# Kernel optimization log

Measured on AMD Instinct MI355X. Metric: run time of the kernel, lower is better.

The kernel has to match this reference:

```python
import jax, jax.numpy as jnp
import numpy as np

N = 50000      # nodes
E = 800000     # edges (avg degree 16)
G = 8          # graphs in batch
D = 128        # in/hidden feats
C = 10         # classes


def setup_inputs() -> dict:
    key = jax.random.key(0)
    ks = jax.random.split(key, 9)
    x = jax.random.normal(ks[0], (N, D), dtype=jnp.float32)
    edge_index = jax.random.randint(ks[1], (2, E), 0, N)
    node2graph = jnp.sort(jax.random.randint(ks[2], (N,), 0, G))
    s = 1.0 / np.sqrt(D)
    W1 = jax.random.normal(ks[3], (D, D), dtype=jnp.float32) * s
    b1 = jnp.zeros((D,), jnp.float32)
    W2 = jax.random.normal(ks[4], (D, D), dtype=jnp.float32) * s
    b2 = jnp.zeros((D,), jnp.float32)
    Wl = jax.random.normal(ks[5], (D, C), dtype=jnp.float32) * s
    bl = jnp.zeros((C,), jnp.float32)
    return {"x": x, "edge_index": edge_index, "node2graph": node2graph,
            "W1": W1, "b1": b1, "W2": W2, "b2": b2, "Wl": Wl, "bl": bl}


def _graph_conv(h, src, dst, out_isqrt, in_isqrt, W, b):
    # DGL GraphConv, norm='both': D_in^{-1/2} A D_out^{-1/2} (h W) + b
    h = (h * out_isqrt[:, None]) @ W
    agg = jax.ops.segment_sum(h[src], dst, num_segments=N)  # SpMM gather/scatter
    return agg * in_isqrt[:, None] + b


def reference(x, edge_index, node2graph, W1, b1, W2, b2, Wl, bl):
    src, dst = edge_index[0], edge_index[1]
    ones_e = jnp.ones((E,), jnp.float32)
    out_deg = jnp.clip(jax.ops.segment_sum(ones_e, src, num_segments=N), 1.0)
    in_deg = jnp.clip(jax.ops.segment_sum(ones_e, dst, num_segments=N), 1.0)
    out_isqrt = jax.lax.rsqrt(out_deg)
    in_isqrt = jax.lax.rsqrt(in_deg)

    h = jax.nn.relu(_graph_conv(x, src, dst, out_isqrt, in_isqrt, W1, b1))
    h = jax.nn.relu(_graph_conv(h, src, dst, out_isqrt, in_isqrt, W2, b2))

    # AvgPooling: per-graph mean of node features
    sums = jax.ops.segment_sum(h, node2graph, num_segments=G)
    counts = jnp.clip(jax.ops.segment_sum(jnp.ones((N,), jnp.float32), node2graph, num_segments=G), 1.0)
    hg = sums / counts[:, None]

    logits = hg @ Wl + bl
    return jax.nn.softmax(logits, axis=1)
```

## Files before the change

kernel.cpp:

```cpp
#include <hip/hip_runtime.h>
#include <stdint.h>

#define FD 128
#define NG 8
#define NC 10
#define MAXB 1024
#define CHUNK 4096
#define BFPAD 4

typedef __attribute__((ext_vector_type(8))) short bf16x8;
typedef __attribute__((ext_vector_type(4))) float f32x4;
typedef __attribute__((ext_vector_type(2))) float f32x2;

__device__ __forceinline__ float bf2f(uint16_t u){
    union { uint32_t i; float f; } v; v.i = ((uint32_t)u) << 16; return v.f;
}
__device__ __forceinline__ uint16_t f2bf(float f){
    union { float f; uint32_t i; } v; v.f = f;
    uint32_t r = v.i + 0x7fff + ((v.i >> 16) & 1);
    return (uint16_t)(r >> 16);
}

#if __has_builtin(__builtin_amdgcn_cvt_pk_f32_fp8) && __has_builtin(__builtin_amdgcn_cvt_pk_fp8_f32)
__device__ __forceinline__ f32x2 fp8lo2f(uint32_t p){
    return __builtin_amdgcn_cvt_pk_f32_fp8((int)p, false);
}
__device__ __forceinline__ f32x2 fp8hi2f(uint32_t p){
    return __builtin_amdgcn_cvt_pk_f32_fp8((int)p, true);
}
__device__ __forceinline__ uint32_t pk4fp8(float a, float b, float c, float d){
    int u = 0;
    u = __builtin_amdgcn_cvt_pk_fp8_f32(a, b, u, false);
    u = __builtin_amdgcn_cvt_pk_fp8_f32(c, d, u, true);
    return (uint32_t)u;
}
#else
__device__ __forceinline__ float fp8tof(uint32_t b){
    union { uint32_t i; float f; } v;
    v.i = ((b & 0x7f) << 20) | ((b & 0x80) << 24);
    return v.f * 0x1p120f;
}
__device__ __forceinline__ f32x2 fp8lo2f(uint32_t p){
    return (f32x2){fp8tof(p & 0xff), fp8tof((p >> 8) & 0xff)};
}
__device__ __forceinline__ f32x2 fp8hi2f(uint32_t p){
    return (f32x2){fp8tof((p >> 16) & 0xff), fp8tof((p >> 24) & 0xff)};
}
__device__ __forceinline__ uint32_t f2fp8(float f){
    union { float f; uint32_t i; } v; v.f = f;
    uint32_t s = (v.i >> 24) & 0x80;
    float a = fabsf(f);
    if (a < 0x1p-10f) return s;
    if (a > 448.f) return s | 0x7e;
    v.f = a;
    uint32_t r = v.i + 0x7ffff + ((v.i >> 20) & 1);
    int e = (int)(r >> 23) - 127 + 7;
    uint32_t m = (r >> 20) & 7;
    if (e <= 0){
        uint32_t q = (uint32_t)(a * 512.f + 0.5f);
        return s | (q > 7 ? 8 : q);
    }
    if (e > 15) return s | 0x7e;
    return s | ((uint32_t)e << 3) | m;
}
__device__ __forceinline__ uint32_t pk4fp8(float a, float b, float c, float d){
    return (uint32_t)f2fp8(a) | ((uint32_t)f2fp8(b)<<8) |
           ((uint32_t)f2fp8(c)<<16) | ((uint32_t)f2fp8(d)<<24);
}
#endif

__global__ __launch_bounds__(256) void k_prep(const float* __restrict__ W1,
        const float* __restrict__ W2, uint16_t* Wf1, uint16_t* Wf2,
        int B, int* __restrict__ bfD, int* __restrict__ bfS,
        float* __restrict__ pool){
    int t = threadIdx.x;
    int id = blockIdx.x*256 + t;
    {
        int w = id >> 14;
        int r = id & 16383;
        int j = r & 7, frag = r >> 3;
        int lane = frag & 63, t2 = frag >> 6;
        int n = t2 & 7, kk = t2 >> 3;
        int k = kk*32 + (lane>>4)*8 + j;
        int col = n*16 + (lane&15);
        float v = (w ? W2 : W1)[k*128 + col];
        (w ? Wf2 : Wf1)[r] = f2bf(v);
    }
    for (int i = id; i < B*BFPAD; i += 32768){ bfD[i] = 0; bfS[i] = 0; }
    if (id < NG*FD) pool[id] = 0.f;
}

__global__ __launch_bounds__(1024) void k_gemm_scatter(const int* __restrict__ ei,
        int E, int B, int shift, int CAP, int C,
        int* __restrict__ bfD, int* __restrict__ bfS,
        uint32_t* __restrict__ tempD, uint16_t* __restrict__ tempS,
        const float* __restrict__ X, const uint16_t* __restrict__ Wf,
        uint8_t* __restrict__ out8, int N){
    __shared__ __align__(16) char lds[45056];
    int t = threadIdx.x;
    int lmask = (1<<shift) - 1;
    if ((int)blockIdx.x < C){
        uint32_t* pay = (uint32_t*)lds;
        int* cnt  = (int*)(lds + 7168*4);
        int* off  = cnt  + MAXB;
        int* resv = off  + MAXB;
        int* scr  = resv + MAXB;
        for (int i=t;i<7168;i+=1024) pay[i] = 0xFFFFFFFFu;
        for (int i=t;i<B;i+=1024) cnt[i] = 0;
        __syncthreads();
        int c = blockIdx.x;
        int e0 = c*CHUNK, e1 = min(E, e0+CHUNK);
        int bb[4], pl[4]; uint32_t val[4];
        #pragma unroll
        for (int k=0;k<4;k++){
            int e = e0 + t + k*1024;
            bb[k] = -1;
            if (e < e1){
                int s = ei[e], d = ei[E+e];
                int b = d >> shift;
                bb[k] = b; val[k] = ((uint32_t)(d & lmask) << 20) | (uint32_t)s;
                pl[k] = atomicAdd(&cnt[b], 1);
            }
        }
        __syncthreads();
        int v = (t < B) ? ((cnt[t]+3) & ~3) : 0;
        scr[t] = v; __syncthreads();
        for (int o=1;o<1024;o<<=1){ int u=(t>=o)?scr[t-o]:0; __syncthreads(); scr[t]+=u; __syncthreads(); }
        if (t < B) off[t] = scr[t] - v;
        __syncthreads();
        int totalPad = scr[1023];
        #pragma unroll
        for (int k=0;k<4;k++)
            if (bb[k] >= 0) pay[off[bb[k]] + pl[k]] = val[k];
        for (int b=t;b<B;b+=1024){
            int pc = (cnt[b]+3) & ~3;
            resv[b] = pc ? atomicAdd(&bfD[b*BFPAD], pc) : 0;
        }
        __syncthreads();
        for (int g=t; g < (totalPad>>2); g += 1024){
            int pos = g << 2;
            int lo = 0, hi = B-1;
            while (lo < hi){ int mid=(lo+hi+1)>>1; if (off[mid] <= pos) lo = mid; else hi = mid-1; }
            int rel = resv[lo] + (pos - off[lo]);
            if (rel + 4 <= CAP){
                uint4 w4 = *(const uint4*)&pay[pos];
                *(uint4*)&tempD[(size_t)lo*CAP + rel] = w4;
            }
        }
        return;
    }
    if ((int)blockIdx.x < 2*C){
        uint16_t* pay = (uint16_t*)lds;
        int* cnt  = (int*)(lds + 11264*2);
        int* off  = cnt  + MAXB;
        int* resv = off  + MAXB;
        int* scr  = resv + MAXB;
        for (int i=t;i<11264;i+=1024) pay[i] = 0xFFFF;
        for (int i=t;i<B;i+=1024) cnt[i] = 0;
        __syncthreads();
        int c = blockIdx.x - C;
        int e0 = c*CHUNK, e1 = min(E, e0+CHUNK);
        int bb[4], pl[4]; uint16_t val[4];
        #pragma unroll
        for (int k=0;k<4;k++){
            int e = e0 + t + k*1024;
            bb[k] = -1;
            if (e < e1){
                int s = ei[e];
                int b = s >> shift;
                bb[k] = b; val[k] = (uint16_t)(s & lmask);
                pl[k] = atomicAdd(&cnt[b], 1);
            }
        }
        __syncthreads();
        int v = (t < B) ? ((cnt[t]+7) & ~7) : 0;
        scr[t] = v; __syncthreads();
        for (int o=1;o<1024;o<<=1){ int u=(t>=o)?scr[t-o]:0; __syncthreads(); scr[t]+=u; __syncthreads(); }
        if (t < B) off[t] = scr[t] - v;
        __syncthreads();
        int totalPad = scr[1023];
        #pragma unroll
        for (int k=0;k<4;k++)
            if (bb[k] >= 0) pay[off[bb[k]] + pl[k]] = val[k];
        for (int b=t;b<B;b+=1024){
            int pc = (cnt[b]+7) & ~7;
            resv[b] = pc ? atomicAdd(&bfS[b*BFPAD], pc) : 0;
        }
        __syncthreads();
        for (int g=t; g < (totalPad>>3); g += 1024){
            int pos = g << 3;
            int lo = 0, hi = B-1;
            while (lo < hi){ int mid=(lo+hi+1)>>1; if (off[mid] <= pos) lo = mid; else hi = mid-1; }
            int rel = resv[lo] + (pos - off[lo]);
            if (rel + 8 <= CAP){
                uint4 w4 = *(const uint4*)&pay[pos];
                *(uint4*)&tempS[(size_t)lo*CAP + rel] = w4;
            }
        }
        return;
    }
    int wave = t>>6, lane = t&63, quad = lane>>4, low = lane&15;
    int rowA  = (blockIdx.x - 2*C)*256 + wave*16 + low;
    int rowAc = min(rowA, N-1);
    const float* arow = X + (size_t)rowAc*FD;
    bf16x8 ah[4];
    #pragma unroll
    for (int kk=0;kk<4;kk++){
        f32x4 f0 = *(const f32x4*)(arow + kk*32 + quad*8);
        f32x4 f1 = *(const f32x4*)(arow + kk*32 + quad*8 + 4);
        #pragma unroll
        for (int j=0;j<4;j++) ah[kk][j]   = (short)f2bf(f0[j]);
        #pragma unroll
        for (int j=0;j<4;j++) ah[kk][j+4] = (short)f2bf(f1[j]);
    }
    f32x4 acc[8];
    #pragma unroll
    for (int n=0;n<8;n++) acc[n] = (f32x4){0.f,0.f,0.f,0.f};
    #pragma unroll
    for (int kk=0;kk<4;kk++){
        #pragma unroll
        for (int n=0;n<8;n++){
            bf16x8 bh = *(const bf16x8*)(Wf + ((size_t)((kk*8+n)*64 + lane))*8);
            acc[n] = __builtin_amdgcn_mfma_f32_16x16x32_bf16(bh, ah[kk], acc[n], 0, 0, 0);
        }
    }
    if (rowA < N){
        uint8_t* orow = out8 + (size_t)rowA*FD;
        #pragma unroll
        for (int n=0;n<8;n++){
            uint32_t pk = pk4fp8(acc[n][0], acc[n][1], acc[n][2], acc[n][3]);
            *(uint32_t*)(orow + n*16 + quad*4) = pk;
        }
    }
}

__global__ __launch_bounds__(256) void k_build(const uint32_t* __restrict__ tempD,
        const uint16_t* __restrict__ tempS,
        const int* __restrict__ bfD, const int* __restrict__ bfS,
        int B, int shift, int N, int CAP,
        int* __restrict__ row_off, int* __restrict__ deg_in,
        float* __restrict__ isqo, int* __restrict__ csr){
    __shared__ int cnt_[MAXB];
    __shared__ int off_[MAXB];
    int b = blockIdx.x, t = threadIdx.x;
    int range = 1<<shift, nb0 = b<<shift;
    int fill = min(bfD[b*BFPAD], CAP);
    const uint32_t* seg = tempD + (size_t)b*CAP;
    for (int i=t;i<range;i+=256) cnt_[i]=0;
    __syncthreads();
    for (int i=t;i<fill;i+=256){
        int loc = (int)(seg[i] >> 20);
        if (loc < range) atomicAdd(&cnt_[loc], 1);
    }
    __syncthreads();
    if (range == 64){
        if (t < 64){
            int v = cnt_[t];
            int inc = v;
            #pragma unroll
            for (int o=1;o<64;o<<=1){
                int u = __shfl_up(inc, o);
                if (t >= o) inc += u;
            }
            off_[t] = inc - v;
        }
    } else if (t == 0){
        int run = 0;
        for (int i=0;i<range;i++){ off_[i]=run; run+=cnt_[i]; }
    }
    __syncthreads();
    int base = b*CAP;
    for (int i=t;i<range;i+=256){
        int node = nb0 + i;
        if (node < N){
            row_off[node] = base + off_[i];
            deg_in[node]  = cnt_[i];
        }
    }
    __syncthreads();
    int* csrb = csr + (size_t)base;
    for (int i=t;i<fill;i+=256){
        uint32_t v = seg[i];
        int loc = (int)(v >> 20);
        if (loc < range){
            int p = atomicAdd(&off_[loc], 1);
            csrb[p] = (int)(v & 0xFFFFFu);
        }
    }
    __syncthreads();
    for (int i=t;i<range;i+=256) cnt_[i]=0;
    __syncthreads();
    int fillS = min(bfS[b*BFPAD], CAP);
    const uint16_t* segS = tempS + (size_t)b*CAP;
    for (int i=t;i<fillS;i+=256){
        int v = (int)segS[i];
        if (v < range) atomicAdd(&cnt_[v], 1);
    }
    __syncthreads();
    for (int i=t;i<range;i+=256){
        int node = nb0 + i;
        if (node < N) isqo[node] = rsqrtf((float)max(cnt_[i], 1));
    }
}

template<bool WSCALE>
__device__ __forceinline__ void spmm_row(const uint2* __restrict__ tp,
        const int* __restrict__ csr_src, const float* __restrict__ isqo,
        int e0, int e1, int l, int qb,
        f32x2& a01, f32x2& a23, f32x2& a45, f32x2& a67){
    for (int base = e0; base < e1; base += 16){
        int my = 0;
        if (base + l < e1) my = csr_src[base + l];
        int cnt = min(16, e1 - base);
        for (int j0 = 0; j0 < cnt; j0 += 8){
            int ss[8];
            #pragma unroll
            for (int k=0;k<8;k++)
                ss[k] = __shfl(my, qb + min(j0 + k, cnt-1));
            uint2 p[8]; float w[8];
            #pragma unroll
            for (int k=0;k<8;k++)
                p[k] = tp[(size_t)ss[k]*16 + l];
            if (WSCALE){
                #pragma unroll
                for (int k=0;k<8;k++) w[k] = isqo[ss[k]];
            }
            #pragma unroll
            for (int k=0;k<8;k++){
                if (j0 + k < cnt){
                    if (WSCALE){
                        a01 += fp8lo2f(p[k].x)*w[k]; a23 += fp8hi2f(p[k].x)*w[k];
                        a45 += fp8lo2f(p[k].y)*w[k]; a67 += fp8hi2f(p[k].y)*w[k];
                    } else {
                        a01 += fp8lo2f(p[k].x); a23 += fp8hi2f(p[k].x);
                        a45 += fp8lo2f(p[k].y); a67 += fp8hi2f(p[k].y);
                    }
                }
            }
        }
    }
}

__global__ __launch_bounds__(256) void k_spmm_gemm(const uint8_t* __restrict__ tmp8,
        const int* __restrict__ row_off, const int* __restrict__ deg_in,
        const int* __restrict__ csr_src, const float* __restrict__ isqo,
        const float* __restrict__ bias, const uint16_t* __restrict__ Wf,
        uint8_t* __restrict__ out8, int N){
    __shared__ __align__(16) uint16_t hsrow[64][136];
    int tid = threadIdx.x;
    int l = tid & 15, qid = tid >> 4, qb = (tid & 63) & 48;
    const uint2* tp = (const uint2*)tmp8;
    f32x4 bv0 = *(const f32x4*)(bias + l*8);
    f32x4 bv1 = *(const f32x4*)(bias + l*8 + 4);
    #pragma unroll
    for (int i = 0; i < 4; i++){
        int rowL = qid*4 + i;
        int node = blockIdx.x*64 + rowL;
        int e0 = 0, e1 = 0;
        if (node < N){ e0 = row_off[node]; e1 = e0 + deg_in[node]; }
        f32x2 a01={0.f,0.f}, a23={0.f,0.f}, a45={0.f,0.f}, a67={0.f,0.f};
        spmm_row<true>(tp, csr_src, isqo, e0, e1, l, qb, a01, a23, a45, a67);
        float isq = rsqrtf((float)max(e1 - e0, 1));
        float r0 = fmaxf(a01.x*isq + bv0[0], 0.f);
        float r1 = fmaxf(a01.y*isq + bv0[1], 0.f);
        float r2 = fmaxf(a23.x*isq + bv0[2], 0.f);
        float r3 = fmaxf(a23.y*isq + bv0[3], 0.f);
        float r4 = fmaxf(a45.x*isq + bv1[0], 0.f);
        float r5 = fmaxf(a45.y*isq + bv1[1], 0.f);
        float r6 = fmaxf(a67.x*isq + bv1[2], 0.f);
        float r7 = fmaxf(a67.y*isq + bv1[3], 0.f);
        uint4 o;
        o.x = (uint32_t)f2bf(r0) | ((uint32_t)f2bf(r1) << 16);
        o.y = (uint32_t)f2bf(r2) | ((uint32_t)f2bf(r3) << 16);
        o.z = (uint32_t)f2bf(r4) | ((uint32_t)f2bf(r5) << 16);
        o.w = (uint32_t)f2bf(r6) | ((uint32_t)f2bf(r7) << 16);
        if (node >= N) o = (uint4){0u,0u,0u,0u};
        *(uint4*)(&hsrow[rowL][l*8]) = o;
    }
    __syncthreads();
    int wave = tid>>6, lane = tid&63, quad = lane>>4, low = lane&15;
    int rowL = wave*16 + low;
    int rowA = blockIdx.x*64 + rowL;
    bf16x8 ah[4];
    #pragma unroll
    for (int kk=0;kk<4;kk++)
        ah[kk] = *(const bf16x8*)(&hsrow[rowL][kk*32 + quad*8]);
    f32x4 acc[8];
    #pragma unroll
    for (int n=0;n<8;n++) acc[n] = (f32x4){0.f,0.f,0.f,0.f};
    #pragma unroll
    for (int kk=0;kk<4;kk++){
        #pragma unroll
        for (int n=0;n<8;n++){
            bf16x8 bh = *(const bf16x8*)(Wf + ((size_t)((kk*8+n)*64 + lane))*8);
            acc[n] = __builtin_amdgcn_mfma_f32_16x16x32_bf16(bh, ah[kk], acc[n], 0, 0, 0);
        }
    }
    if (rowA < N){
        float sc = isqo[rowA];
        uint8_t* orow = out8 + (size_t)rowA*FD;
        #pragma unroll
        for (int n=0;n<8;n++){
            uint32_t pk = pk4fp8(acc[n][0]*sc, acc[n][1]*sc, acc[n][2]*sc, acc[n][3]*sc);
            *(uint32_t*)(orow + n*16 + quad*4) = pk;
        }
    }
}

__global__ __launch_bounds__(256) void k_spmm_pool(const uint8_t* __restrict__ tmp8,
        const int* __restrict__ row_off, const int* __restrict__ deg_in,
        const int* __restrict__ csr_src,
        const float* __restrict__ bias, const int* __restrict__ n2g,
        float* __restrict__ pool, int N){
    __shared__ float sacc[NG*FD];
    int tid = threadIdx.x;
    for (int i = tid; i < NG*FD; i += 256) sacc[i] = 0.f;
    __syncthreads();
    int l = tid & 15, qid = tid >> 4, qb = (tid & 63) & 48;
    const uint2* tp = (const uint2*)tmp8;
    f32x4 bv0 = *(const f32x4*)(bias + l*8);
    f32x4 bv1 = *(const f32x4*)(bias + l*8 + 4);
    int rg = -1;
    float racc[8];
    #pragma unroll
    for (int j=0;j<8;j++) racc[j] = 0.f;
    #pragma unroll
    for (int i = 0; i < 4; i++){
        int node = blockIdx.x*64 + qid*4 + i;
        if (node < N){
            int e0 = row_off[node], e1 = e0 + deg_in[node];
            f32x2 a01={0.f,0.f}, a23={0.f,0.f}, a45={0.f,0.f}, a67={0.f,0.f};
            spmm_row<false>(tp, csr_src, nullptr, e0, e1, l, qb, a01, a23, a45, a67);
            float isq = rsqrtf((float)max(e1 - e0, 1));
            float r[8];
            r[0] = fmaxf(a01.x*isq + bv0[0], 0.f);
            r[1] = fmaxf(a01.y*isq + bv0[1], 0.f);
            r[2] = fmaxf(a23.x*isq + bv0[2], 0.f);
            r[3] = fmaxf(a23.y*isq + bv0[3], 0.f);
            r[4] = fmaxf(a45.x*isq + bv1[0], 0.f);
            r[5] = fmaxf(a45.y*isq + bv1[1], 0.f);
            r[6] = fmaxf(a67.x*isq + bv1[2], 0.f);
            r[7] = fmaxf(a67.y*isq + bv1[3], 0.f);
            int g = n2g[node];
            if (g != rg){
                if (rg >= 0){
                    #pragma unroll
                    for (int j=0;j<8;j++) atomicAdd(&sacc[rg*FD + l*8 + j], racc[j]);
                }
                rg = g;
                #pragma unroll
                for (int j=0;j<8;j++) racc[j] = 0.f;
            }
            #pragma unroll
            for (int j=0;j<8;j++) racc[j] += r[j];
        }
    }
    if (rg >= 0){
        #pragma unroll
        for (int j=0;j<8;j++) atomicAdd(&sacc[rg*FD + l*8 + j], racc[j]);
    }
    __syncthreads();
    for (int i = tid; i < NG*FD; i += 256){
        float v = sacc[i];
        if (v != 0.f) atomicAdd(&pool[i], v);
    }
}

__global__ __launch_bounds__(128) void k_final(const float* __restrict__ pool,
        const int* __restrict__ n2g, int N, const float* __restrict__ Wl,
        const float* __restrict__ bl, float* __restrict__ out){
    __shared__ int ub[NG+1];
    __shared__ float logits[NG][NC];
    int t = threadIdx.x;
    if (t <= NG){
        int lo = 0, hi = N;
        while (lo < hi){ int mid = (lo+hi)>>1; if (n2g[mid] < t) lo = mid+1; else hi = mid; }
        ub[t] = lo;
    }
    __syncthreads();
    if (t < NG*NC){
        int g = t/NC, c = t%NC;
        float cnt = (float)max(ub[g+1]-ub[g], 1);
        float inv = 1.f/cnt;
        float acc = bl[c];
        for (int d=0; d<FD; d++)
            acc += pool[g*FD+d]*inv * Wl[d*NC+c];
        logits[g][c] = acc;
    }
    __syncthreads();
    if (t < NG*NC){
        int g = t/NC, c = t%NC;
        float m = -1e30f;
        for (int i=0;i<NC;i++) m = fmaxf(m, logits[g][i]);
        float ssum = 0.f;
        for (int i=0;i<NC;i++) ssum += expf(logits[g][i]-m);
        out[t] = expf(logits[g][c]-m)/ssum;
    }
}

extern "C" void kernel_launch(void* const* d_in, const int* in_sizes, int n_in,
                              void* d_out, int out_size, void* d_ws, size_t ws_size,
                              hipStream_t stream) {
    const float* x   = (const float*)d_in[0];
    const int*   ei  = (const int*)d_in[1];
    const int*   n2g = (const int*)d_in[2];
    const float* W1  = (const float*)d_in[3];
    const float* b1  = (const float*)d_in[4];
    const float* W2  = (const float*)d_in[5];
    const float* b2  = (const float*)d_in[6];
    const float* Wl  = (const float*)d_in[7];
    const float* bl  = (const float*)d_in[8];
    float* outp = (float*)d_out;

    int N = in_sizes[2];
    int E = in_sizes[1] / 2;

    int shift = 6;
    while ((((N + (1<<shift) - 1) >> shift) > MAXB) && shift < 10) shift++;
    int B = (N + (1<<shift) - 1) >> shift;
    int C = (E + CHUNK - 1) / CHUNK;
    int meanFill = (int)(((long long)E << shift) / (N > 0 ? N : 1)) + 1;
    int CAP = 4096;
    while (CAP < 3*meanFill) CAP <<= 1;

    char* w = (char*)d_ws;
    size_t off = 0;
    auto alloc = [&](size_t bytes)->char*{ char* p = w + off; off += (bytes + 255) & ~(size_t)255; return p; };
    float*    pool    = (float*)alloc((size_t)NG*FD*4);
    int*      deg_in  = (int*)alloc((size_t)N*4);
    int*      row_off = (int*)alloc((size_t)N*4);
    float*    isqo    = (float*)alloc((size_t)N*4);
    int*      bfD     = (int*)alloc((size_t)MAXB*BFPAD*4);
    int*      bfS     = (int*)alloc((size_t)MAXB*BFPAD*4);
    uint16_t* Wf1     = (uint16_t*)alloc(16384*2);
    uint16_t* Wf2     = (uint16_t*)alloc(16384*2);
    uint32_t* tempD   = (uint32_t*)alloc((size_t)B*CAP*4);
    uint16_t* tempS   = (uint16_t*)alloc((size_t)B*CAP*2);
    int*      csr     = (int*)alloc((size_t)B*CAP*4);
    uint8_t*  tmp8    = (uint8_t*)alloc((size_t)N*FD);
    uint8_t*  tmp8b   = (uint8_t*)alloc((size_t)N*FD);
    (void)ws_size;

    int gb2 = (N + 255)/256;
    int gb  = (N + 63)/64;

    k_prep        <<<128,         256,  0, stream>>>(W1, W2, Wf1, Wf2, B, bfD, bfS, pool);
    k_gemm_scatter<<<2*C + gb2,   1024, 0, stream>>>(ei, E, B, shift, CAP, C,
                                                     bfD, bfS, tempD, tempS,
                                                     x, Wf1, tmp8, N);
    k_build       <<<B,           256,  0, stream>>>(tempD, tempS, bfD, bfS, B, shift, N, CAP,
                                                     row_off, deg_in, isqo, csr);
    k_spmm_gemm   <<<gb,          256,  0, stream>>>(tmp8,  row_off, deg_in, csr, isqo, b1, Wf2, tmp8b, N);
    k_spmm_pool   <<<gb,          256,  0, stream>>>(tmp8b, row_off, deg_in, csr, b2, n2g, pool, N);
    k_final       <<<1,           128,  0, stream>>>(pool, n2g, N, Wl, bl, outp);
}
```

Measured before the change: 197.9 us.

## Quantize intermediate node features to per-row scaled FP4 for SpMM gathers

Stores the transformed node features as 4-bit E2M1 values with a per-row scale instead of FP8. This halves the bytes gathered per edge in both SpMM passes, and the per-row scale is folded into per-node weight tables (wtab1/wtab2) used during aggregation. The SpMM kernels also drop from 64 to 32 rows per block, with occupancy hints, and the second GEMM splits output columns across waves, using an LDS atomicMax to find each row's maximum. The cost is much coarser quantization and some extra encode/decode ALU work, which risks accuracy.

```diff
diff --git a/kernel.cpp b/kernel.cpp
--- a/kernel.cpp
+++ b/kernel.cpp
@@ -21,51 +21,35 @@
     return (uint16_t)(r >> 16);
 }
 
-#if __has_builtin(__builtin_amdgcn_cvt_pk_f32_fp8) && __has_builtin(__builtin_amdgcn_cvt_pk_fp8_f32)
-__device__ __forceinline__ f32x2 fp8lo2f(uint32_t p){
-    return __builtin_amdgcn_cvt_pk_f32_fp8((int)p, false);
-}
-__device__ __forceinline__ f32x2 fp8hi2f(uint32_t p){
-    return __builtin_amdgcn_cvt_pk_f32_fp8((int)p, true);
-}
-__device__ __forceinline__ uint32_t pk4fp8(float a, float b, float c, float d){
-    int u = 0;
-    u = __builtin_amdgcn_cvt_pk_fp8_f32(a, b, u, false);
-    u = __builtin_amdgcn_cvt_pk_fp8_f32(c, d, u, true);
-    return (uint32_t)u;
+__device__ __forceinline__ uint32_t enc4(float v, float s){
+    float a = fabsf(v)*s;
+    uint32_t c = (uint32_t)((a>=0.25f)+(a>=0.75f)+(a>=1.25f)+(a>=1.75f)
+                           +(a>=2.5f)+(a>=3.5f)+(a>=5.f));
+    return c | ((__float_as_uint(v)>>28) & 8u);
+}
+#if __has_builtin(__builtin_amdgcn_cvt_scalef32_pk_f32_fp4)
+__device__ __forceinline__ void acc_fp4(uint32_t p, float w,
+        f32x2& a01, f32x2& a23, f32x2& a45, f32x2& a67){
+    f32x2 d;
+    d = __builtin_amdgcn_cvt_scalef32_pk_f32_fp4(p, 1.0f, 0); a01.x += d.x*w; a01.y += d.y*w;
+    d = __builtin_amdgcn_cvt_scalef32_pk_f32_fp4(p, 1.0f, 1); a23.x += d.x*w; a23.y += d.y*w;
+    d = __builtin_amdgcn_cvt_scalef32_pk_f32_fp4(p, 1.0f, 2); a45.x += d.x*w; a45.y += d.y*w;
+    d = __builtin_amdgcn_cvt_scalef32_pk_f32_fp4(p, 1.0f, 3); a67.x += d.x*w; a67.y += d.y*w;
 }
 #else
-__device__ __forceinline__ float fp8tof(uint32_t b){
-    union { uint32_t i; float f; } v;
-    v.i = ((b & 0x7f) << 20) | ((b & 0x80) << 24);
-    return v.f * 0x1p120f;
-}
-__device__ __forceinline__ f32x2 fp8lo2f(uint32_t p){
-    return (f32x2){fp8tof(p & 0xff), fp8tof((p >> 8) & 0xff)};
-}
-__device__ __forceinline__ f32x2 fp8hi2f(uint32_t p){
-    return (f32x2){fp8tof((p >> 16) & 0xff), fp8tof((p >> 24) & 0xff)};
-}
-__device__ __forceinline__ uint32_t f2fp8(float f){
-    union { float f; uint32_t i; } v; v.f = f;
-    uint32_t s = (v.i >> 24) & 0x80;
-    float a = fabsf(f);
-    if (a < 0x1p-10f) return s;
-    if (a > 448.f) return s | 0x7e;
-    v.f = a;
-    uint32_t r = v.i + 0x7ffff + ((v.i >> 20) & 1);
-    int e = (int)(r >> 23) - 127 + 7;
-    uint32_t m = (r >> 20) & 7;
-    if (e <= 0){
-        uint32_t q = (uint32_t)(a * 512.f + 0.5f);
-        return s | (q > 7 ? 8 : q);
-    }
-    if (e > 15) return s | 0x7e;
-    return s | ((uint32_t)e << 3) | m;
-}
-__device__ __forceinline__ uint32_t pk4fp8(float a, float b, float c, float d){
-    return (uint32_t)f2fp8(a) | ((uint32_t)f2fp8(b)<<8) |
-           ((uint32_t)f2fp8(c)<<16) | ((uint32_t)f2fp8(d)<<24);
+__device__ __forceinline__ float dec4(uint32_t n, float w){
+    uint32_t c = n & 7u;
+    uint32_t bits = (c >= 2u) ? (0x3F000000u + (c << 22)) : ((c & 1u) ? 0x3F000000u : 0u);
+    bits |= (n & 8u) << 28;
+    union { uint32_t u; float f; } v; v.u = bits;
+    return v.f * w;
+}
+__device__ __forceinline__ void acc_fp4(uint32_t p, float w,
+        f32x2& a01, f32x2& a23, f32x2& a45, f32x2& a67){
+    a01.x += dec4(p & 15u, w);        a01.y += dec4((p>>4) & 15u, w);
+    a23.x += dec4((p>>8) & 15u, w);   a23.y += dec4((p>>12) & 15u, w);
+    a45.x += dec4((p>>16) & 15u, w);  a45.y += dec4((p>>20) & 15u, w);
+    a67.x += dec4((p>>24) & 15u, w);  a67.y += dec4(p>>28, w);
 }
 #endif
 
@@ -95,7 +79,7 @@
         int* __restrict__ bfD, int* __restrict__ bfS,
         uint32_t* __restrict__ tempD, uint16_t* __restrict__ tempS,
         const float* __restrict__ X, const uint16_t* __restrict__ Wf,
-        uint8_t* __restrict__ out8, int N){
+        uint8_t* __restrict__ out4, float* __restrict__ rsc1, int N){
     __shared__ __align__(16) char lds[45056];
     int t = threadIdx.x;
     int lmask = (1<<shift) - 1;
@@ -224,13 +208,24 @@
             acc[n] = __builtin_amdgcn_mfma_f32_16x16x32_bf16(bh, ah[kk], acc[n], 0, 0, 0);
         }
     }
+    float m = 0.f;
+    #pragma unroll
+    for (int n=0;n<8;n++){
+        #pragma unroll
+        for (int j=0;j<4;j++) m = fmaxf(m, fabsf(acc[n][j]));
+    }
+    m = fmaxf(m, __shfl_xor(m, 16));
+    m = fmaxf(m, __shfl_xor(m, 32));
+    float s = (m > 0.f) ? 6.f/m : 0.f;
     if (rowA < N){
-        uint8_t* orow = out8 + (size_t)rowA*FD;
+        uint8_t* orow = out4 + (size_t)rowA*64;
         #pragma unroll
         for (int n=0;n<8;n++){
-            uint32_t pk = pk4fp8(acc[n][0], acc[n][1], acc[n][2], acc[n][3]);
-            *(uint32_t*)(orow + n*16 + quad*4) = pk;
-        }
+            uint32_t h = enc4(acc[n][0],s) | (enc4(acc[n][1],s)<<4)
+                       | (enc4(acc[n][2],s)<<8) | (enc4(acc[n][3],s)<<12);
+            *(uint16_t*)(orow + n*8 + quad*2) = (uint16_t)h;
+        }
+        if (quad == 0) rsc1[rowA] = m * (1.f/6.f);
     }
 }
 
@@ -239,7 +234,9 @@
         const int* __restrict__ bfD, const int* __restrict__ bfS,
         int B, int shift, int N, int CAP,
         int* __restrict__ row_off, int* __restrict__ deg_in,
-        float* __restrict__ isqo, int* __restrict__ csr){
+        const float* __restrict__ rsc1,
+        float* __restrict__ isqo, float* __restrict__ wtab1,
+        int* __restrict__ csr){
     __shared__ int cnt_[MAXB];
     __shared__ int off_[MAXB];
     int b = blockIdx.x, t = threadIdx.x;
@@ -299,13 +296,16 @@
     __syncthreads();
     for (int i=t;i<range;i+=256){
         int node = nb0 + i;
-        if (node < N) isqo[node] = rsqrtf((float)max(cnt_[i], 1));
-    }
-}
-
-template<bool WSCALE>
-__device__ __forceinline__ void spmm_row(const uint2* __restrict__ tp,
-        const int* __restrict__ csr_src, const float* __restrict__ isqo,
+        if (node < N){
+            float iq = rsqrtf((float)max(cnt_[i], 1));
+            isqo[node]  = iq;
+            wtab1[node] = iq * rsc1[node];
+        }
+    }
+}
+
+__device__ __forceinline__ void spmm_row4(const uint32_t* __restrict__ tp,
+        const int* __restrict__ csr_src, const float* __restrict__ wt,
         int e0, int e1, int l, int qb,
         f32x2& a01, f32x2& a23, f32x2& a45, f32x2& a67){
     for (int base = e0; base < e1; base += 16){
@@ -317,49 +317,44 @@
             #pragma unroll
             for (int k=0;k<8;k++)
                 ss[k] = __shfl(my, qb + min(j0 + k, cnt-1));
-            uint2 p[8]; float w[8];
+            uint32_t p[8]; float w[8];
             #pragma unroll
             for (int k=0;k<8;k++)
                 p[k] = tp[(size_t)ss[k]*16 + l];
-            if (WSCALE){
-                #pragma unroll
-                for (int k=0;k<8;k++) w[k] = isqo[ss[k]];
-            }
+            #pragma unroll
+            for (int k=0;k<8;k++)
+                w[k] = wt[ss[k]];
             #pragma unroll
             for (int k=0;k<8;k++){
-                if (j0 + k < cnt){
-                    if (WSCALE){
-                        a01 += fp8lo2f(p[k].x)*w[k]; a23 += fp8hi2f(p[k].x)*w[k];
-                        a45 += fp8lo2f(p[k].y)*w[k]; a67 += fp8hi2f(p[k].y)*w[k];
-                    } else {
-                        a01 += fp8lo2f(p[k].x); a23 += fp8hi2f(p[k].x);
-                        a45 += fp8lo2f(p[k].y); a67 += fp8hi2f(p[k].y);
-                    }
-                }
-            }
-        }
-    }
-}
-
-__global__ __launch_bounds__(256) void k_spmm_gemm(const uint8_t* __restrict__ tmp8,
+                if (j0 + k < cnt)
+                    acc_fp4(p[k], w[k], a01, a23, a45, a67);
+            }
+        }
+    }
+}
+
+__global__ __launch_bounds__(256, 6) void k_spmm_gemm(const uint8_t* __restrict__ tmp4a,
         const int* __restrict__ row_off, const int* __restrict__ deg_in,
-        const int* __restrict__ csr_src, const float* __restrict__ isqo,
+        const int* __restrict__ csr_src, const float* __restrict__ wtab1,
+        const float* __restrict__ isqo,
         const float* __restrict__ bias, const uint16_t* __restrict__ Wf,
-        uint8_t* __restrict__ out8, int N){
-    __shared__ __align__(16) uint16_t hsrow[64][136];
+        uint8_t* __restrict__ out4, float* __restrict__ wtab2, int N){
+    __shared__ __align__(16) uint16_t hsrow[32][136];
+    __shared__ uint32_t rmax[32];
     int tid = threadIdx.x;
+    if (tid < 32) rmax[tid] = 0u;
     int l = tid & 15, qid = tid >> 4, qb = (tid & 63) & 48;
-    const uint2* tp = (const uint2*)tmp8;
+    const uint32_t* tp = (const uint32_t*)tmp4a;
     f32x4 bv0 = *(const f32x4*)(bias + l*8);
     f32x4 bv1 = *(const f32x4*)(bias + l*8 + 4);
     #pragma unroll
-    for (int i = 0; i < 4; i++){
-        int rowL = qid*4 + i;
-        int node = blockIdx.x*64 + rowL;
+    for (int i = 0; i < 2; i++){
+        int rowL = qid*2 + i;
+        int node = blockIdx.x*32 + rowL;
         int e0 = 0, e1 = 0;
         if (node < N){ e0 = row_off[node]; e1 = e0 + deg_in[node]; }
         f32x2 a01={0.f,0.f}, a23={0.f,0.f}, a45={0.f,0.f}, a67={0.f,0.f};
-        spmm_row<true>(tp, csr_src, isqo, e0, e1, l, qb, a01, a23, a45, a67);
+        spmm_row4(tp, csr_src, wtab1, e0, e1, l, qb, a01, a23, a45, a67);
         float isq = rsqrtf((float)max(e1 - e0, 1));
         float r0 = fmaxf(a01.x*isq + bv0[0], 0.f);
         float r1 = fmaxf(a01.y*isq + bv0[1], 0.f);
@@ -379,37 +374,51 @@
     }
     __syncthreads();
     int wave = tid>>6, lane = tid&63, quad = lane>>4, low = lane&15;
-    int rowL = wave*16 + low;
-    int rowA = blockIdx.x*64 + rowL;
+    int rowL = (wave&1)*16 + low;
+    int rowA = blockIdx.x*32 + rowL;
+    int nb0 = (wave>>1)*4;
     bf16x8 ah[4];
     #pragma unroll
     for (int kk=0;kk<4;kk++)
         ah[kk] = *(const bf16x8*)(&hsrow[rowL][kk*32 + quad*8]);
-    f32x4 acc[8];
-    #pragma unroll
-    for (int n=0;n<8;n++) acc[n] = (f32x4){0.f,0.f,0.f,0.f};
+    f32x4 acc[4];
+    #pragma unroll
+    for (int n=0;n<4;n++) acc[n] = (f32x4){0.f,0.f,0.f,0.f};
     #pragma unroll
     for (int kk=0;kk<4;kk++){
         #pragma unroll
-        for (int n=0;n<8;n++){
+        for (int n2=0;n2<4;n2++){
+            int n = nb0 + n2;
             bf16x8 bh = *(const bf16x8*)(Wf + ((size_t)((kk*8+n)*64 + lane))*8);
-            acc[n] = __builtin_amdgcn_mfma_f32_16x16x32_bf16(bh, ah[kk], acc[n], 0, 0, 0);
-        }
-    }
+            acc[n2] = __builtin_amdgcn_mfma_f32_16x16x32_bf16(bh, ah[kk], acc[n2], 0, 0, 0);
+        }
+    }
+    float pm = 0.f;
+    #pragma unroll
+    for (int n2=0;n2<4;n2++){
+        #pragma unroll
+        for (int j=0;j<4;j++) pm = fmaxf(pm, fabsf(acc[n2][j]));
+    }
+    atomicMax(&rmax[rowL], __float_as_uint(pm));
+    __syncthreads();
+    float m = __uint_as_float(rmax[rowL]);
+    float s = (m > 0.f) ? 6.f/m : 0.f;
     if (rowA < N){
-        float sc = isqo[rowA];
-        uint8_t* orow = out8 + (size_t)rowA*FD;
-        #pragma unroll
-        for (int n=0;n<8;n++){
-            uint32_t pk = pk4fp8(acc[n][0]*sc, acc[n][1]*sc, acc[n][2]*sc, acc[n][3]*sc);
-            *(uint32_t*)(orow + n*16 + quad*4) = pk;
-        }
-    }
-}
-
-__global__ __launch_bounds__(256) void k_spmm_pool(const uint8_t* __restrict__ tmp8,
+        uint8_t* orow = out4 + (size_t)rowA*64;
+        #pragma unroll
+        for (int n2=0;n2<4;n2++){
+            int n = nb0 + n2;
+            uint32_t h = enc4(acc[n2][0],s) | (enc4(acc[n2][1],s)<<4)
+                       | (enc4(acc[n2][2],s)<<8) | (enc4(acc[n2][3],s)<<12);
+            *(uint16_t*)(orow + n*8 + quad*2) = (uint16_t)h;
+        }
+        if (nb0 == 0 && quad == 0) wtab2[rowA] = isqo[rowA] * m * (1.f/6.f);
+    }
+}
+
+__global__ __launch_bounds__(256, 6) void k_spmm_pool(const uint8_t* __restrict__ tmp4b,
         const int* __restrict__ row_off, const int* __restrict__ deg_in,
-        const int* __restrict__ csr_src,
+        const int* __restrict__ csr_src, const float* __restrict__ wtab2,
         const float* __restrict__ bias, const int* __restrict__ n2g,
         float* __restrict__ pool, int N){
     __shared__ float sacc[NG*FD];
@@ -417,7 +426,7 @@
     for (int i = tid; i < NG*FD; i += 256) sacc[i] = 0.f;
     __syncthreads();
     int l = tid & 15, qid = tid >> 4, qb = (tid & 63) & 48;
-    const uint2* tp = (const uint2*)tmp8;
+    const uint32_t* tp = (const uint32_t*)tmp4b;
     f32x4 bv0 = *(const f32x4*)(bias + l*8);
     f32x4 bv1 = *(const f32x4*)(bias + l*8 + 4);
     int rg = -1;
@@ -425,12 +434,12 @@
     #pragma unroll
     for (int j=0;j<8;j++) racc[j] = 0.f;
     #pragma unroll
-    for (int i = 0; i < 4; i++){
-        int node = blockIdx.x*64 + qid*4 + i;
+    for (int i = 0; i < 2; i++){
+        int node = blockIdx.x*32 + qid*2 + i;
         if (node < N){
             int e0 = row_off[node], e1 = e0 + deg_in[node];
             f32x2 a01={0.f,0.f}, a23={0.f,0.f}, a45={0.f,0.f}, a67={0.f,0.f};
-            spmm_row<false>(tp, csr_src, nullptr, e0, e1, l, qb, a01, a23, a45, a67);
+            spmm_row4(tp, csr_src, wtab2, e0, e1, l, qb, a01, a23, a45, a67);
             float isq = rsqrtf((float)max(e1 - e0, 1));
             float r[8];
             r[0] = fmaxf(a01.x*isq + bv0[0], 0.f);
@@ -530,6 +539,9 @@
     int*      deg_in  = (int*)alloc((size_t)N*4);
     int*      row_off = (int*)alloc((size_t)N*4);
     float*    isqo    = (float*)alloc((size_t)N*4);
+    float*    rsc1    = (float*)alloc((size_t)N*4);
+    float*    wtab1   = (float*)alloc((size_t)N*4);
+    float*    wtab2   = (float*)alloc((size_t)N*4);
     int*      bfD     = (int*)alloc((size_t)MAXB*BFPAD*4);
     int*      bfS     = (int*)alloc((size_t)MAXB*BFPAD*4);
     uint16_t* Wf1     = (uint16_t*)alloc(16384*2);
@@ -537,20 +549,22 @@
     uint32_t* tempD   = (uint32_t*)alloc((size_t)B*CAP*4);
     uint16_t* tempS   = (uint16_t*)alloc((size_t)B*CAP*2);
     int*      csr     = (int*)alloc((size_t)B*CAP*4);
-    uint8_t*  tmp8    = (uint8_t*)alloc((size_t)N*FD);
-    uint8_t*  tmp8b   = (uint8_t*)alloc((size_t)N*FD);
+    uint8_t*  tmp4a   = (uint8_t*)alloc((size_t)N*64);
+    uint8_t*  tmp4b   = (uint8_t*)alloc((size_t)N*64);
     (void)ws_size;
 
     int gb2 = (N + 255)/256;
-    int gb  = (N + 63)/64;
+    int gb  = (N + 31)/32;
 
     k_prep        <<<128,         256,  0, stream>>>(W1, W2, Wf1, Wf2, B, bfD, bfS, pool);
     k_gemm_scatter<<<2*C + gb2,   1024, 0, stream>>>(ei, E, B, shift, CAP, C,
                                                      bfD, bfS, tempD, tempS,
-                                                     x, Wf1, tmp8, N);
+                                                     x, Wf1, tmp4a, rsc1, N);
     k_build       <<<B,           256,  0, stream>>>(tempD, tempS, bfD, bfS, B, shift, N, CAP,
-                                                     row_off, deg_in, isqo, csr);
-    k_spmm_gemm   <<<gb,          256,  0, stream>>>(tmp8,  row_off, deg_in, csr, isqo, b1, Wf2, tmp8b, N);
-    k_spmm_pool   <<<gb,          256,  0, stream>>>(tmp8b, row_off, deg_in, csr, b2, n2g, pool, N);
+                                                     row_off, deg_in, rsc1, isqo, wtab1, csr);
+    k_spmm_gemm   <<<gb,          256,  0, stream>>>(tmp4a, row_off, deg_in, csr, wtab1, isqo,
+                                                     b1, Wf2, tmp4b, wtab2, N);
+    k_spmm_pool   <<<gb,          256,  0, stream>>>(tmp4b, row_off, deg_in, csr, wtab2,
+                                                     b2, n2g, pool, N);
     k_final       <<<1,           128,  0, stream>>>(pool, n2g, N, Wl, bl, outp);
 }
```

Measured after the change: 195.4 us. About the same (-1.3%).

## Merge dst/src bucketing blocks and halve rows per SpMM block

Applied to the files above, without the earlier changes.

The scatter kernel now has each edge-chunk block load src and dst once and run both the dst bucketing and the src bucketing passes in sequence, reusing the LDS. This halves the number of bucketing blocks and avoids reading the edge list twice. Separately, the SpMM+GEMM and SpMM+pool kernels now handle 32 nodes per block instead of 64. In the fused GEMM stage each wave computes half of the output columns, and both kernels get an occupancy hint of 6. The aim is more blocks and better latency hiding for the gather, at the cost of serialising the two bucketing passes inside each block.

```diff
diff --git a/kernel.cpp b/kernel.cpp
--- a/kernel.cpp
+++ b/kernel.cpp
@@ -100,25 +100,32 @@
     int t = threadIdx.x;
     int lmask = (1<<shift) - 1;
     if ((int)blockIdx.x < C){
-        uint32_t* pay = (uint32_t*)lds;
-        int* cnt  = (int*)(lds + 7168*4);
+        uint32_t* payD = (uint32_t*)lds;
+        uint16_t* payS = (uint16_t*)lds;
+        int* cnt  = (int*)(lds + 28672);
         int* off  = cnt  + MAXB;
         int* resv = off  + MAXB;
         int* scr  = resv + MAXB;
-        for (int i=t;i<7168;i+=1024) pay[i] = 0xFFFFFFFFu;
-        for (int i=t;i<B;i+=1024) cnt[i] = 0;
-        __syncthreads();
         int c = blockIdx.x;
         int e0 = c*CHUNK, e1 = min(E, e0+CHUNK);
-        int bb[4], pl[4]; uint32_t val[4];
+        int ss[4], dd[4];
         #pragma unroll
         for (int k=0;k<4;k++){
             int e = e0 + t + k*1024;
+            bool ok = e < e1;
+            ss[k] = ok ? ei[e]   : -1;
+            dd[k] = ok ? ei[E+e] : -1;
+        }
+        for (int i=t;i<7168;i+=1024) payD[i] = 0xFFFFFFFFu;
+        for (int i=t;i<B;i+=1024) cnt[i] = 0;
+        __syncthreads();
+        int bb[4], pl[4];
+        #pragma unroll
+        for (int k=0;k<4;k++){
             bb[k] = -1;
-            if (e < e1){
-                int s = ei[e], d = ei[E+e];
-                int b = d >> shift;
-                bb[k] = b; val[k] = ((uint32_t)(d & lmask) << 20) | (uint32_t)s;
+            if (dd[k] >= 0){
+                int b = dd[k] >> shift;
+                bb[k] = b;
                 pl[k] = atomicAdd(&cnt[b], 1);
             }
         }
@@ -131,7 +138,8 @@
         int totalPad = scr[1023];
         #pragma unroll
         for (int k=0;k<4;k++)
-            if (bb[k] >= 0) pay[off[bb[k]] + pl[k]] = val[k];
+            if (bb[k] >= 0)
+                payD[off[bb[k]] + pl[k]] = ((uint32_t)(dd[k] & lmask) << 20) | (uint32_t)ss[k];
         for (int b=t;b<B;b+=1024){
             int pc = (cnt[b]+3) & ~3;
             resv[b] = pc ? atomicAdd(&bfD[b*BFPAD], pc) : 0;
@@ -143,45 +151,33 @@
             while (lo < hi){ int mid=(lo+hi+1)>>1; if (off[mid] <= pos) lo = mid; else hi = mid-1; }
             int rel = resv[lo] + (pos - off[lo]);
             if (rel + 4 <= CAP){
-                uint4 w4 = *(const uint4*)&pay[pos];
+                uint4 w4 = *(const uint4*)&payD[pos];
                 *(uint4*)&tempD[(size_t)lo*CAP + rel] = w4;
             }
         }
-        return;
-    }
-    if ((int)blockIdx.x < 2*C){
-        uint16_t* pay = (uint16_t*)lds;
-        int* cnt  = (int*)(lds + 11264*2);
-        int* off  = cnt  + MAXB;
-        int* resv = off  + MAXB;
-        int* scr  = resv + MAXB;
-        for (int i=t;i<11264;i+=1024) pay[i] = 0xFFFF;
+        __syncthreads();
+        for (int i=t;i<11264;i+=1024) payS[i] = 0xFFFF;
         for (int i=t;i<B;i+=1024) cnt[i] = 0;
         __syncthreads();
-        int c = blockIdx.x - C;
-        int e0 = c*CHUNK, e1 = min(E, e0+CHUNK);
-        int bb[4], pl[4]; uint16_t val[4];
         #pragma unroll
         for (int k=0;k<4;k++){
-            int e = e0 + t + k*1024;
             bb[k] = -1;
-            if (e < e1){
-                int s = ei[e];
-                int b = s >> shift;
-                bb[k] = b; val[k] = (uint16_t)(s & lmask);
+            if (ss[k] >= 0){
+                int b = ss[k] >> shift;
+                bb[k] = b;
                 pl[k] = atomicAdd(&cnt[b], 1);
             }
         }
         __syncthreads();
-        int v = (t < B) ? ((cnt[t]+7) & ~7) : 0;
+        v = (t < B) ? ((cnt[t]+7) & ~7) : 0;
         scr[t] = v; __syncthreads();
         for (int o=1;o<1024;o<<=1){ int u=(t>=o)?scr[t-o]:0; __syncthreads(); scr[t]+=u; __syncthreads(); }
         if (t < B) off[t] = scr[t] - v;
         __syncthreads();
-        int totalPad = scr[1023];
+        totalPad = scr[1023];
         #pragma unroll
         for (int k=0;k<4;k++)
-            if (bb[k] >= 0) pay[off[bb[k]] + pl[k]] = val[k];
+            if (bb[k] >= 0) payS[off[bb[k]] + pl[k]] = (uint16_t)(ss[k] & lmask);
         for (int b=t;b<B;b+=1024){
             int pc = (cnt[b]+7) & ~7;
             resv[b] = pc ? atomicAdd(&bfS[b*BFPAD], pc) : 0;
@@ -193,14 +189,14 @@
             while (lo < hi){ int mid=(lo+hi+1)>>1; if (off[mid] <= pos) lo = mid; else hi = mid-1; }
             int rel = resv[lo] + (pos - off[lo]);
             if (rel + 8 <= CAP){
-                uint4 w4 = *(const uint4*)&pay[pos];
+                uint4 w4 = *(const uint4*)&payS[pos];
                 *(uint4*)&tempS[(size_t)lo*CAP + rel] = w4;
             }
         }
         return;
     }
     int wave = t>>6, lane = t&63, quad = lane>>4, low = lane&15;
-    int rowA  = (blockIdx.x - 2*C)*256 + wave*16 + low;
+    int rowA  = (blockIdx.x - C)*256 + wave*16 + low;
     int rowAc = min(rowA, N-1);
     const float* arow = X + (size_t)rowAc*FD;
     bf16x8 ah[4];
@@ -341,21 +337,21 @@
     }
 }
 
-__global__ __launch_bounds__(256) void k_spmm_gemm(const uint8_t* __restrict__ tmp8,
+__global__ __launch_bounds__(256, 6) void k_spmm_gemm(const uint8_t* __restrict__ tmp8,
         const int* __restrict__ row_off, const int* __restrict__ deg_in,
         const int* __restrict__ csr_src, const float* __restrict__ isqo,
         const float* __restrict__ bias, const uint16_t* __restrict__ Wf,
         uint8_t* __restrict__ out8, int N){
-    __shared__ __align__(16) uint16_t hsrow[64][136];
+    __shared__ __align__(16) uint16_t hsrow[32][136];
     int tid = threadIdx.x;
     int l = tid & 15, qid = tid >> 4, qb = (tid & 63) & 48;
     const uint2* tp = (const uint2*)tmp8;
     f32x4 bv0 = *(const f32x4*)(bias + l*8);
     f32x4 bv1 = *(const f32x4*)(bias + l*8 + 4);
     #pragma unroll
-    for (int i = 0; i < 4; i++){
-        int rowL = qid*4 + i;
-        int node = blockIdx.x*64 + rowL;
+    for (int i = 0; i < 2; i++){
+        int rowL = qid*2 + i;
+        int node = blockIdx.x*32 + rowL;
         int e0 = 0, e1 = 0;
         if (node < N){ e0 = row_off[node]; e1 = e0 + deg_in[node]; }
         f32x2 a01={0.f,0.f}, a23={0.f,0.f}, a45={0.f,0.f}, a67={0.f,0.f};
@@ -379,35 +375,38 @@
     }
     __syncthreads();
     int wave = tid>>6, lane = tid&63, quad = lane>>4, low = lane&15;
-    int rowL = wave*16 + low;
-    int rowA = blockIdx.x*64 + rowL;
+    int rowL = (wave&1)*16 + low;
+    int rowA = blockIdx.x*32 + rowL;
+    int nb0 = (wave>>1)*4;
     bf16x8 ah[4];
     #pragma unroll
     for (int kk=0;kk<4;kk++)
         ah[kk] = *(const bf16x8*)(&hsrow[rowL][kk*32 + quad*8]);
-    f32x4 acc[8];
-    #pragma unroll
-    for (int n=0;n<8;n++) acc[n] = (f32x4){0.f,0.f,0.f,0.f};
+    f32x4 acc[4];
+    #pragma unroll
+    for (int n=0;n<4;n++) acc[n] = (f32x4){0.f,0.f,0.f,0.f};
     #pragma unroll
     for (int kk=0;kk<4;kk++){
         #pragma unroll
-        for (int n=0;n<8;n++){
+        for (int n2=0;n2<4;n2++){
+            int n = nb0 + n2;
             bf16x8 bh = *(const bf16x8*)(Wf + ((size_t)((kk*8+n)*64 + lane))*8);
-            acc[n] = __builtin_amdgcn_mfma_f32_16x16x32_bf16(bh, ah[kk], acc[n], 0, 0, 0);
+            acc[n2] = __builtin_amdgcn_mfma_f32_16x16x32_bf16(bh, ah[kk], acc[n2], 0, 0, 0);
         }
     }
     if (rowA < N){
         float sc = isqo[rowA];
         uint8_t* orow = out8 + (size_t)rowA*FD;
         #pragma unroll
-        for (int n=0;n<8;n++){
-            uint32_t pk = pk4fp8(acc[n][0]*sc, acc[n][1]*sc, acc[n][2]*sc, acc[n][3]*sc);
+        for (int n2=0;n2<4;n2++){
+            int n = nb0 + n2;
+            uint32_t pk = pk4fp8(acc[n2][0]*sc, acc[n2][1]*sc, acc[n2][2]*sc, acc[n2][3]*sc);
             *(uint32_t*)(orow + n*16 + quad*4) = pk;
         }
     }
 }
 
-__global__ __launch_bounds__(256) void k_spmm_pool(const uint8_t* __restrict__ tmp8,
+__global__ __launch_bounds__(256, 6) void k_spmm_pool(const uint8_t* __restrict__ tmp8,
         const int* __restrict__ row_off, const int* __restrict__ deg_in,
         const int* __restrict__ csr_src,
         const float* __restrict__ bias, const int* __restrict__ n2g,
@@ -425,8 +424,8 @@
     #pragma unroll
     for (int j=0;j<8;j++) racc[j] = 0.f;
     #pragma unroll
-    for (int i = 0; i < 4; i++){
-        int node = blockIdx.x*64 + qid*4 + i;
+    for (int i = 0; i < 2; i++){
+        int node = blockIdx.x*32 + qid*2 + i;
         if (node < N){
             int e0 = row_off[node], e1 = e0 + deg_in[node];
             f32x2 a01={0.f,0.f}, a23={0.f,0.f}, a45={0.f,0.f}, a67={0.f,0.f};
@@ -542,15 +541,15 @@
     (void)ws_size;
 
     int gb2 = (N + 255)/256;
-    int gb  = (N + 63)/64;
-
-    k_prep        <<<128,         256,  0, stream>>>(W1, W2, Wf1, Wf2, B, bfD, bfS, pool);
-    k_gemm_scatter<<<2*C + gb2,   1024, 0, stream>>>(ei, E, B, shift, CAP, C,
-                                                     bfD, bfS, tempD, tempS,
-                                                     x, Wf1, tmp8, N);
-    k_build       <<<B,           256,  0, stream>>>(tempD, tempS, bfD, bfS, B, shift, N, CAP,
-                                                     row_off, deg_in, isqo, csr);
-    k_spmm_gemm   <<<gb,          256,  0, stream>>>(tmp8,  row_off, deg_in, csr, isqo, b1, Wf2, tmp8b, N);
-    k_spmm_pool   <<<gb,          256,  0, stream>>>(tmp8b, row_off, deg_in, csr, b2, n2g, pool, N);
-    k_final       <<<1,           128,  0, stream>>>(pool, n2g, N, Wl, bl, outp);
-}
+    int gb  = (N + 31)/32;
+
+    k_prep        <<<128,       256,  0, stream>>>(W1, W2, Wf1, Wf2, B, bfD, bfS, pool);
+    k_gemm_scatter<<<C + gb2,   1024, 0, stream>>>(ei, E, B, shift, CAP, C,
+                                                   bfD, bfS, tempD, tempS,
+                                                   x, Wf1, tmp8, N);
+    k_build       <<<B,         256,  0, stream>>>(tempD, tempS, bfD, bfS, B, shift, N, CAP,
+                                                   row_off, deg_in, isqo, csr);
+    k_spmm_gemm   <<<gb,        256,  0, stream>>>(tmp8,  row_off, deg_in, csr, isqo, b1, Wf2, tmp8b, N);
+    k_spmm_pool   <<<gb,        256,  0, stream>>>(tmp8b, row_off, deg_in, csr, b2, n2g, pool, N);
+    k_final       <<<1,         128,  0, stream>>>(pool, n2g, N, Wl, bl, outp);
+}
```

Result: faster. 187.6 us (-5.2%).
